# Kernel tuning notes

Measured on AMD Instinct MI355X. Metric: run time of the kernel, lower is better.

Reference implementation:

```python
import jax, jax.numpy as jnp
import numpy as np

EPS_LN = 1e-5

def _layernorm(x, g, b):
    mu = jnp.mean(x, axis=-1, keepdims=True)
    var = jnp.mean((x - mu) ** 2, axis=-1, keepdims=True)
    return (x - mu) * jax.lax.rsqrt(var + EPS_LN) * g + b


def setup_inputs() -> dict:
    B, S, D = 8, 2048, 512
    key = jax.random.key(0)
    ks = jax.random.split(key, 12)
    s = 1.0 / np.sqrt(D)
    inp = {
        "x": jax.random.normal(ks[0], (B, S, D), dtype=jnp.float32),
        "ln1_g": jnp.ones((D,), jnp.float32),
        "ln1_b": jnp.zeros((D,), jnp.float32),
        "ln2_g": jnp.ones((D,), jnp.float32),
        "ln2_b": jnp.zeros((D,), jnp.float32),
        "Wq": jax.random.normal(ks[1], (D, D), jnp.float32) * s,
        "bq": jnp.zeros((D,), jnp.float32),
        "Wk": jax.random.normal(ks[2], (D, D), jnp.float32) * s,
        "bk": jnp.zeros((D,), jnp.float32),
        "Wv": jax.random.normal(ks[3], (D, D), jnp.float32) * s,
        "bv": jnp.zeros((D,), jnp.float32),
        "Wi": jax.random.normal(ks[4], (D, D), jnp.float32) * s,
        "bi": jnp.zeros((D,), jnp.float32),
        "Wf": jax.random.normal(ks[5], (D, D), jnp.float32) * s,
        "bf": jnp.zeros((D,), jnp.float32),
        "Wo": jax.random.normal(ks[6], (D, D), jnp.float32) * s,
        "bo": jnp.zeros((D,), jnp.float32),
        "W1": jax.random.normal(ks[7], (D, 4 * D), jnp.float32) * s,
        "b1": jnp.zeros((4 * D,), jnp.float32),
        "W2": jax.random.normal(ks[8], (4 * D, D), jnp.float32) * (1.0 / np.sqrt(4 * D)),
        "b2": jnp.zeros((D,), jnp.float32),
    }
    return inp


def reference(x, ln1_g, ln1_b, ln2_g, ln2_b, Wq, bq, Wk, bk, Wv, bv,
              Wi, bi, Wf, bf, Wo, bo, W1, b1, W2, b2):
    B, S, D = x.shape
    normed = _layernorm(x, ln1_g, ln1_b)                      # [B,S,D]
    # All projections depend only on x -> batch them over time.
    q = normed @ Wq + bq
    k = (normed @ Wk + bk) / jnp.sqrt(jnp.float32(D))
    v = normed @ Wv + bv
    it = normed @ Wi + bi
    ft = normed @ Wf + bf
    o = jax.nn.sigmoid(normed @ Wo + bo)

    def tm(a):  # time-major [S,B,D]
        return jnp.swapaxes(a, 0, 1)

    def step(carry, xs):
        C, n, m = carry
        q_t, k_t, v_t, it_t, ft_t, o_t = xs
        m_new = jnp.maximum(ft_t + m, it_t)
        i_g = jnp.exp(it_t - m_new)
        f_g = jnp.exp(ft_t + m - m_new)
        # outer(v,k): [B,D,1]*[B,1,D]
        C_new = f_g[..., None] * C + i_g[..., None] * (v_t[:, :, None] * k_t[:, None, :])
        n_new = f_g * n + i_g * k_t
        h = o_t * jnp.einsum('bij,bj->bi', C_new, q_t)
        return (C_new, n_new, m_new), h

    C0 = jnp.zeros((B, D, D), x.dtype)
    n0 = jnp.zeros((B, D), x.dtype)
    m0 = jnp.zeros((B, D), x.dtype)
    (_, _, _), h_seq = jax.lax.scan(step, (C0, n0, m0),
                                    (tm(q), tm(k), tm(v), tm(it), tm(ft), tm(o)))
    h = jnp.swapaxes(h_seq, 0, 1)                             # [B,S,D]

    out = x + h
    ffn_in = _layernorm(out, ln2_g, ln2_b)
    ffn = jax.nn.gelu(ffn_in @ W1 + b1, approximate=False) @ W2 + b2
    return out + ffn
```

## Files before the change

kernel.cpp:

```cpp
#include <hip/hip_runtime.h>
#include <hip/hip_bf16.h>
#include <cstdint>

typedef unsigned short u16;
typedef unsigned int u32;
typedef __attribute__((ext_vector_type(8))) short short8;
typedef __attribute__((ext_vector_type(4))) float f32x4;

#define NB 8
#define NS 2048
#define ND 512
#define NM (NB * NS)
#define CL 64
#define NCH (NS / CL)
#define CL2 128
#define NCH2 (NS / CL2)
static constexpr size_t BSDn = (size_t)NM * ND;
#define KSCALE 0.044194173824159216f

#define OFF_QB ((size_t)0)
#define OFF_KB (BSDn * 2)
#define OFF_KT (BSDn * 4)
#define OFF_VT (BSDn * 6)
#define OFF_OT (BSDn * 8)
#define OFF_IT (BSDn * 10)
#define OFF_FT (BSDn * 14)
#define OFF_G  (BSDn * 18)
#define OFF_GO (BSDn * 18 + ((size_t)2 << 20))
#define OFF_AC (BSDn * 18 + ((size_t)3 << 20))
#define OFF_X  (OFF_AC + ((size_t)32 << 20))
#define OFF_UB (OFF_X + ((size_t)16 << 20))
#define OFF_GA (OFF_UB + ((size_t)16 << 20))
#define OFF_END (OFF_GA + ((size_t)1 << 20))

typedef __attribute__((address_space(1))) const u32 gas_u32;
typedef __attribute__((address_space(3))) u32 las_u32;

__device__ __forceinline__ u16 f2bf(float f) {
    u32 i = __builtin_bit_cast(u32, f);
    u32 r = i + 0x7FFFu + ((i >> 16) & 1u);
    return (u16)(r >> 16);
}
__device__ __forceinline__ float bf2f(u16 h) {
    return __builtin_bit_cast(float, (u32)h << 16);
}

__device__ __forceinline__ void lds_barrier() {
    __builtin_amdgcn_sched_barrier(0);
    asm volatile("s_waitcnt lgkmcnt(0)" ::: "memory");
    __builtin_amdgcn_s_barrier();
    __builtin_amdgcn_sched_barrier(0);
}

__global__ __launch_bounds__(256) void wcorr_kernel(
        const float* __restrict__ Wi, const float* __restrict__ Wf,
        u16* __restrict__ WT) {
    int idx = blockIdx.x * 256 + threadIdx.x;
    int n = idx / 1536, k = idx - n * 1536;
    const float* Wp = (n >> 9) ? Wf : Wi;
    int d = n & 511;
    u16 o;
    if (k < 1024) {
        o = f2bf(Wp[(size_t)(k & 511) * 512 + d]);
    } else {
        float w = Wp[(size_t)(k - 1024) * 512 + d];
        o = f2bf(w - bf2f(f2bf(w)));
    }
    WT[idx] = o;
}

__global__ __launch_bounds__(256) void wconv_kernel(const float* __restrict__ W,
        u16* __restrict__ WT, int lk, int N, int total) {
    int idx = blockIdx.x * 256 + threadIdx.x;
    if (idx >= total) return;
    int n = idx >> lk;
    int k = idx & ((1 << lk) - 1);
    WT[idx] = f2bf(W[(size_t)k * N + n]);
}

__global__ __launch_bounds__(256) void bias_concat_kernel(
        const float* b0, const float* b1, const float* b2,
        const float* b3, const float* b4, const float* b5,
        float* __restrict__ ball) {
    int idx = blockIdx.x * 256 + threadIdx.x;
    if (idx >= 3072) return;
    int p = idx >> 9, d = idx & 511;
    float v;
    switch (p) {
        case 0: v = b0[d]; break;
        case 1: v = b1[d]; break;
        case 2: v = b2[d]; break;
        case 3: v = b3[d]; break;
        case 4: v = b4[d]; break;
        default: v = b5[d]; break;
    }
    ball[idx] = v;
}

__global__ __launch_bounds__(256) void ln1_kernel(const float* __restrict__ x,
        const float* __restrict__ g, const float* __restrict__ bb,
        u16* __restrict__ nout) {
    int wave = threadIdx.x >> 6, lane = threadIdx.x & 63;
    size_t row = (size_t)blockIdx.x * 4 + wave;
    const float* xr = x + row * ND + lane * 8;
    float4 a0 = *(const float4*)xr;
    float4 a1 = *(const float4*)(xr + 4);
    float xs[8] = {a0.x, a0.y, a0.z, a0.w, a1.x, a1.y, a1.z, a1.w};
    float s = 0.f;
#pragma unroll
    for (int u = 0; u < 8; ++u) s += xs[u];
#pragma unroll
    for (int off = 32; off; off >>= 1) s += __shfl_xor(s, off);
    float mu = s * (1.0f / ND);
    float ss = 0.f;
#pragma unroll
    for (int u = 0; u < 8; ++u) { xs[u] -= mu; ss += xs[u] * xs[u]; }
#pragma unroll
    for (int off = 32; off; off >>= 1) ss += __shfl_xor(ss, off);
    float rs = rsqrtf(ss * (1.0f / ND) + 1e-5f);
    const float* gp = g + lane * 8;
    const float* bp = bb + lane * 8;
    float4 g0 = *(const float4*)gp, g1 = *(const float4*)(gp + 4);
    float4 c0 = *(const float4*)bp, c1 = *(const float4*)(bp + 4);
    float gg[8] = {g0.x, g0.y, g0.z, g0.w, g1.x, g1.y, g1.z, g1.w};
    float cc[8] = {c0.x, c0.y, c0.z, c0.w, c1.x, c1.y, c1.z, c1.w};
    u32 owh[4], owl[4];
#pragma unroll
    for (int u = 0; u < 4; ++u) {
        float y0 = xs[2 * u] * rs * gg[2 * u] + cc[2 * u];
        float y1 = xs[2 * u + 1] * rs * gg[2 * u + 1] + cc[2 * u + 1];
        u16 h0 = f2bf(y0), h1 = f2bf(y1);
        u16 l0 = f2bf(y0 - bf2f(h0)), l1 = f2bf(y1 - bf2f(h1));
        owh[u] = (u32)h0 | ((u32)h1 << 16);
        owl[u] = (u32)l0 | ((u32)l1 << 16);
    }
    u16* rb = nout + row * 1024;
    *(uint4*)(rb + lane * 8) = make_uint4(owh[0], owh[1], owh[2], owh[3]);
    *(uint4*)(rb + 512 + lane * 8) = make_uint4(owl[0], owl[1], owl[2], owl[3]);
}

__global__ __launch_bounds__(256) void resid_ln2_kernel(const float* __restrict__ x,
        const float* __restrict__ h, const float* __restrict__ g,
        const float* __restrict__ bb, float* __restrict__ outb,
        u16* __restrict__ fin) {
    int wave = threadIdx.x >> 6, lane = threadIdx.x & 63;
    size_t row = (size_t)blockIdx.x * 4 + wave;
    const float* xr = x + row * ND + lane * 8;
    const float* hr = h + row * ND + lane * 8;
    float4 a0 = *(const float4*)xr;
    float4 a1 = *(const float4*)(xr + 4);
    float4 h0 = *(const float4*)hr;
    float4 h1 = *(const float4*)(hr + 4);
    float xs[8] = {a0.x + h0.x, a0.y + h0.y, a0.z + h0.z, a0.w + h0.w,
                   a1.x + h1.x, a1.y + h1.y, a1.z + h1.z, a1.w + h1.w};
    float* orow = outb + row * ND + lane * 8;
    *(float4*)orow = make_float4(xs[0], xs[1], xs[2], xs[3]);
    *(float4*)(orow + 4) = make_float4(xs[4], xs[5], xs[6], xs[7]);
    float s = 0.f;
#pragma unroll
    for (int u = 0; u < 8; ++u) s += xs[u];
#pragma unroll
    for (int off = 32; off; off >>= 1) s += __shfl_xor(s, off);
    float mu = s * (1.0f / ND);
    float ss = 0.f;
#pragma unroll
    for (int u = 0; u < 8; ++u) { xs[u] -= mu; ss += xs[u] * xs[u]; }
#pragma unroll
    for (int off = 32; off; off >>= 1) ss += __shfl_xor(ss, off);
    float rs = rsqrtf(ss * (1.0f / ND) + 1e-5f);
    const float* gp = g + lane * 8;
    const float* bp = bb + lane * 8;
    float4 g0 = *(const float4*)gp, g1 = *(const float4*)(gp + 4);
    float4 c0 = *(const float4*)bp, c1 = *(const float4*)(bp + 4);
    float gg[8] = {g0.x, g0.y, g0.z, g0.w, g1.x, g1.y, g1.z, g1.w};
    float cc[8] = {c0.x, c0.y, c0.z, c0.w, c1.x, c1.y, c1.z, c1.w};
    u32 ow[4];
#pragma unroll
    for (int u = 0; u < 4; ++u) {
        float y0 = xs[2 * u] * rs * gg[2 * u] + cc[2 * u];
        float y1 = xs[2 * u + 1] * rs * gg[2 * u + 1] + cc[2 * u + 1];
        ow[u] = (u32)f2bf(y0) | ((u32)f2bf(y1) << 16);
    }
    *(uint4*)(fin + row * ND + lane * 8) = make_uint4(ow[0], ow[1], ow[2], ow[3]);
}

__global__ __launch_bounds__(256) void gqk_kernel(
        const u16* __restrict__ Qb, const u16* __restrict__ Kb,
        u16* __restrict__ Gm) {
    __shared__ u16 Qs[64][520];
    __shared__ u16 Ks[64][520];
    int tid = threadIdx.x;
    int w = tid >> 6, lane = tid & 63;
    int b = blockIdx.x >> 5, c = blockIdx.x & 31;
    int t0 = c * CL;
    {
        int row = tid >> 2, cb = (tid & 3) * 128;
        const u16* qsrc = Qb + ((size_t)b * NS + t0 + row) * ND + cb;
        const u16* ksrc = Kb + ((size_t)b * NS + t0 + row) * ND + cb;
#pragma unroll
        for (int u = 0; u < 16; ++u) {
            *(short8*)&Qs[row][cb + u * 8] = *(const short8*)(qsrc + u * 8);
            *(short8*)&Ks[row][cb + u * 8] = *(const short8*)(ksrc + u * 8);
        }
    }
    __syncthreads();
    int qw = lane & 15, kg = lane >> 4;
    f32x4 ga[4];
#pragma unroll
    for (int ns = 0; ns < 4; ++ns) ga[ns] = (f32x4){0.f, 0.f, 0.f, 0.f};
    for (int kb = 0; kb < 16; ++kb) {
        short8 aq = *(const short8*)&Qs[(w << 4) + qw][kb * 32 + (kg << 3)];
#pragma unroll
        for (int ns = 0; ns < 4; ++ns) {
            short8 bk = *(const short8*)&Ks[(ns << 4) + qw][kb * 32 + (kg << 3)];
            ga[ns] = __builtin_amdgcn_mfma_f32_16x16x32_bf16(aq, bk, ga[ns], 0, 0, 0);
        }
    }
    u16* gout = Gm + (size_t)(b * NCH + c) * CL * CL;
#pragma unroll
    for (int ns = 0; ns < 4; ++ns) {
#pragma unroll
        for (int rg = 0; rg < 4; ++rg) {
            int t = (w << 4) + (kg << 2) + rg;
            int s = (ns << 4) + qw;
            gout[t * CL + s] = (s <= t) ? f2bf(ga[ns][rg]) : (u16)0;
        }
    }
}

__global__ __launch_bounds__(256) void gqkoff_kernel(
        const u16* __restrict__ Qb, const u16* __restrict__ Kb,
        u16* __restrict__ Go) {
    __shared__ u16 Qs[64][520];
    __shared__ u16 Ks[64][520];
    int tid = threadIdx.x;
    int w = tid >> 6, lane = tid & 63;
    int b = blockIdx.x >> 4, c = blockIdx.x & 15;
    int t0q = c * CL2 + 64, t0k = c * CL2;
    {
        int row = tid >> 2, cb = (tid & 3) * 128;
        const u16* qsrc = Qb + ((size_t)b * NS + t0q + row) * ND + cb;
        const u16* ksrc = Kb + ((size_t)b * NS + t0k + row) * ND + cb;
#pragma unroll
        for (int u = 0; u < 16; ++u) {
            *(short8*)&Qs[row][cb + u * 8] = *(const short8*)(qsrc + u * 8);
            *(short8*)&Ks[row][cb + u * 8] = *(const short8*)(ksrc + u * 8);
        }
    }
    __syncthreads();
    int qw = lane & 15, kg = lane >> 4;
    f32x4 ga[4];
#pragma unroll
    for (int ns = 0; ns < 4; ++ns) ga[ns] = (f32x4){0.f, 0.f, 0.f, 0.f};
    for (int kb = 0; kb < 16; ++kb) {
        short8 aq = *(const short8*)&Qs[(w << 4) + qw][kb * 32 + (kg << 3)];
#pragma unroll
        for (int ns = 0; ns < 4; ++ns) {
            short8 bk = *(const short8*)&Ks[(ns << 4) + qw][kb * 32 + (kg << 3)];
            ga[ns] = __builtin_amdgcn_mfma_f32_16x16x32_bf16(aq, bk, ga[ns], 0, 0, 0);
        }
    }
    u16* gout = Go + (size_t)(b * NCH2 + c) * CL * CL;
#pragma unroll
    for (int ns = 0; ns < 4; ++ns) {
#pragma unroll
        for (int rg = 0; rg < 4; ++rg) {
            int t = (w << 4) + (kg << 2) + rg;
            int s = (ns << 4) + qw;
            gout[t * CL + s] = f2bf(ga[ns][rg]);
        }
    }
}

__global__ __launch_bounds__(128) void gates_kernel(
        const float* __restrict__ IT, const float* __restrict__ FT,
        const u16* __restrict__ VT,
        u16* __restrict__ A1g, u16* __restrict__ A2g,
        u16* __restrict__ Ubg, float* __restrict__ gamg) {
    int w = threadIdx.x >> 6, lane = threadIdx.x & 63;
    int rp = blockIdx.x & 7;
    int bl = blockIdx.x >> 3;
    int b = bl >> 5, isl = bl & 31;
    int il = rp * 2 + w;
    int i = (isl << 4) + il;
    size_t rowb = ((size_t)b * ND + i) * NS;
    size_t tb = (size_t)bl * 32768 + il * 128;
    float mo = 0.f;
    for (int c = 0; c < NCH2; ++c) {
        size_t g0 = rowb + c * CL2 + lane;
        float ft0 = FT[g0], it0 = IT[g0], v0 = bf2f(VT[g0]);
        float ft1 = FT[g0 + 64], it1 = IT[g0 + 64], v1 = bf2f(VT[g0 + 64]);
        float bs0 = ft0;
#pragma unroll
        for (int o = 1; o < 64; o <<= 1) {
            float nv = __shfl_up(bs0, o);
            if (lane >= o) bs0 += nv;
        }
        float e0 = it0 - bs0;
        float M0 = e0;
#pragma unroll
        for (int o = 1; o < 64; o <<= 1) {
            float nv = __shfl_up(M0, o);
            if (lane >= o) M0 = fmaxf(M0, nv);
        }
        M0 = fmaxf(M0, mo);
        float M0t = __shfl(M0, 63);
        float bs0t = __shfl(bs0, 63);
        float bs1 = ft1;
#pragma unroll
        for (int o = 1; o < 64; o <<= 1) {
            float nv = __shfl_up(bs1, o);
            if (lane >= o) bs1 += nv;
        }
        bs1 += bs0t;
        float e1 = it1 - bs1;
        float M1 = e1;
#pragma unroll
        for (int o = 1; o < 64; o <<= 1) {
            float nv = __shfl_up(M1, o);
            if (lane >= o) M1 = fmaxf(M1, nv);
        }
        M1 = fmaxf(M1, M0t);
        float E = __shfl(M1, 63);
        float bst = __shfl(bs1, 63);
        size_t oofs = tb + (size_t)c * 2048 + lane;
        Ubg[oofs] = f2bf(__expf(e0 - E) * v0);
        A1g[oofs] = f2bf(__expf(mo - M0));
        A2g[oofs] = f2bf(__expf(fminf(E - M0, 80.f)));
        Ubg[oofs + 64] = f2bf(__expf(e1 - E) * v1);
        A1g[oofs + 64] = f2bf(__expf(mo - M1));
        A2g[oofs + 64] = f2bf(__expf(fminf(E - M1, 80.f)));
        if (lane == 0) gamg[((size_t)bl * NCH2 + c) * 16 + il] = __expf(mo - E);
        mo = bst + E;
    }
}

__global__ __launch_bounds__(512) void recur_kernel(
        const u16* __restrict__ Qb, const u16* __restrict__ KT,
        const u16* __restrict__ Gd, const u16* __restrict__ Go,
        const u16* __restrict__ A1g, const u16* __restrict__ A2g,
        const u16* __restrict__ Ubg, const float* __restrict__ gamg,
        const u16* __restrict__ OT, float* __restrict__ H) {
    __shared__ u16 Chi[2][16][520];
    __shared__ u16 Ubl[2][16][136];
    __shared__ u16 A1l[2][16][136];
    __shared__ u16 A2l[2][16][136];
    __shared__ float gaml[2][16];
    int tid = threadIdx.x;
    int w = tid >> 6, lane = tid & 63;
    int hb = w >> 2, tl16 = w & 3;
    int b = blockIdx.x & 7;
    int isl = blockIdx.x >> 3;
    int i0 = isl << 4;
    int qw = lane & 15, kg = lane >> 4;
    f32x4 cacc[4];
#pragma unroll
    for (int n = 0; n < 4; ++n) cacc[n] = (f32x4){0.f, 0.f, 0.f, 0.f};

    size_t bT = (size_t)b * NS;
    size_t bD = (size_t)b * ND;
    size_t gt2 = (size_t)(b * 32 + isl) * 32768;
    int grow = tid >> 5;
    int gquad = (tid & 31) << 2;

    const u16* qpf = Qb + (bT + w * 16 + qw) * ND + (kg << 3);
    const u16* kpf = KT + (bD + w * 64 + qw) * NS + (kg << 3);
    const u16* gdp = Gd + ((size_t)(b * 32 + hb) * 4096)
                     + (size_t)(tl16 * 16 + qw) * 64 + (kg << 3);
    const u16* gop = Go + ((size_t)(b * 16) * 4096)
                     + (size_t)(tl16 * 16 + qw) * 64 + (kg << 3);
    const u16* ubp = Ubg + gt2 + grow * 128 + gquad;
    const u16* a1p = A1g + gt2 + grow * 128 + gquad;
    const u16* a2p = A2g + gt2 + grow * 128 + gquad;
    const float* gamp = gamg + (size_t)(b * 32 + isl) * (NCH2 * 16) + tid;
    const u16* otp = OT + (bD + i0 + qw) * NS + w * 16 + (kg << 2);

    uint2 nub = make_uint2(0, 0), na1 = make_uint2(0, 0), na2 = make_uint2(0, 0);
    float ngam = 0.f;
    auto issue_gates = [&]() {
        nub = *(const uint2*)ubp; ubp += 2048;
        na1 = *(const uint2*)a1p; a1p += 2048;
        na2 = *(const uint2*)a2p; a2p += 2048;
        if (tid < 16) ngam = *gamp;
        gamp += 16;
    };
    issue_gates();

    for (int c = 0; c < NCH2; ++c) {
        int buf = c & 1;
        int t0 = c * CL2;
        short8 nq[16], nk[16], ngd[2], ngo[2];
#pragma unroll
        for (int kk = 0; kk < 16; ++kk) nq[kk] = *(const short8*)(qpf + kk * 32);
        qpf += CL2 * ND;
#pragma unroll
        for (int kb = 0; kb < 4; ++kb)
#pragma unroll
            for (int n = 0; n < 4; ++n)
                nk[kb * 4 + n] = *(const short8*)(kpf + (size_t)(n << 4) * NS + kb * 32);
        kpf += CL2;
        ngd[0] = *(const short8*)gdp;
        ngd[1] = *(const short8*)(gdp + 32);
        gdp += 2 * 4096;
        if (hb == 1) {
            ngo[0] = *(const short8*)gop;
            ngo[1] = *(const short8*)(gop + 32);
        }
        gop += 4096;
        uint2 cov = *(const uint2*)otp;
        otp += CL2;
        uint2 cub = nub, ca1 = na1, ca2 = na2;
        float cgam = ngam;
        if (c + 1 < NCH2) issue_gates();

        *(uint2*)&Ubl[buf][grow][gquad] = cub;
        *(uint2*)&A1l[buf][grow][gquad] = ca1;
        *(uint2*)&A2l[buf][grow][gquad] = ca2;
        if (tid < 16) gaml[buf][tid] = cgam;
#pragma unroll
        for (int n = 0; n < 4; ++n) {
            int j = (w << 6) + (n << 4) + qw;
#pragma unroll
            for (int rg = 0; rg < 4; ++rg)
                Chi[buf][(kg << 2) + rg][j] = f2bf(cacc[n][rg]);
        }
        lds_barrier();

        f32x4 qc0 = (f32x4){0.f, 0.f, 0.f, 0.f};
        f32x4 qc1 = (f32x4){0.f, 0.f, 0.f, 0.f};
#pragma unroll
        for (int kk = 0; kk < 8; ++kk) {
            short8 b0 = *(const short8*)&Chi[buf][qw][(2 * kk) * 32 + (kg << 3)];
            short8 b1_ = *(const short8*)&Chi[buf][qw][(2 * kk + 1) * 32 + (kg << 3)];
            qc0 = __builtin_amdgcn_mfma_f32_16x16x32_bf16(nq[2 * kk], b0, qc0, 0, 0, 0);
            qc1 = __builtin_amdgcn_mfma_f32_16x16x32_bf16(nq[2 * kk + 1], b1_, qc1, 0, 0, 0);
        }
        f32x4 pin = (f32x4){0.f, 0.f, 0.f, 0.f};
        if (hb == 0) {
#pragma unroll
            for (int kb = 0; kb < 2; ++kb) {
                short8 bu = *(const short8*)&Ubl[buf][qw][kb * 32 + (kg << 3)];
                pin = __builtin_amdgcn_mfma_f32_16x16x32_bf16(ngd[kb], bu, pin, 0, 0, 0);
            }
        } else {
#pragma unroll
            for (int kb = 0; kb < 2; ++kb) {
                short8 bu = *(const short8*)&Ubl[buf][qw][kb * 32 + (kg << 3)];
                pin = __builtin_amdgcn_mfma_f32_16x16x32_bf16(ngo[kb], bu, pin, 0, 0, 0);
            }
#pragma unroll
            for (int kb = 0; kb < 2; ++kb) {
                short8 bu = *(const short8*)&Ubl[buf][qw][64 + kb * 32 + (kg << 3)];
                pin = __builtin_amdgcn_mfma_f32_16x16x32_bf16(ngd[kb], bu, pin, 0, 0, 0);
            }
        }
        {
            float g[4];
#pragma unroll
            for (int rg = 0; rg < 4; ++rg) g[rg] = gaml[buf][(kg << 2) + rg];
#pragma unroll
            for (int n = 0; n < 4; ++n) {
#pragma unroll
                for (int rg = 0; rg < 4; ++rg) cacc[n][rg] *= g[rg];
            }
#pragma unroll
            for (int kb = 0; kb < 4; ++kb) {
                short8 au = *(const short8*)&Ubl[buf][qw][kb * 32 + (kg << 3)];
#pragma unroll
                for (int n = 0; n < 4; ++n)
                    cacc[n] = __builtin_amdgcn_mfma_f32_16x16x32_bf16(
                            au, nk[kb * 4 + n], cacc[n], 0, 0, 0);
            }
        }
        {
            float ov[4];
            ov[0] = bf2f((u16)(cov.x & 0xffff));
            ov[1] = bf2f((u16)(cov.x >> 16));
            ov[2] = bf2f((u16)(cov.y & 0xffff));
            ov[3] = bf2f((u16)(cov.y >> 16));
#pragma unroll
            for (int rg = 0; rg < 4; ++rg) {
                int tl = w * 16 + (kg << 2) + rg;
                float a1v = bf2f(A1l[buf][qw][tl]);
                float a2v = bf2f(A2l[buf][qw][tl]);
                float qc = qc0[rg] + qc1[rg];
                H[(bT + t0 + tl) * ND + i0 + qw] = ov[rg] * (a1v * qc + a2v * pin[rg]);
            }
        }
    }
}

template <int MODE>
__global__ __launch_bounds__(256) void gemm_kernel(
        const u16* __restrict__ A, const u16* __restrict__ BT,
        int M, int N, int K, int lda, int ldb, int kwrap,
        const float* __restrict__ bias,
        char* __restrict__ pb,
        float* __restrict__ outf, u16* __restrict__ outh,
        const float* __restrict__ resid) {
    __shared__ u16 As[2][128 * 32];
    __shared__ u16 Bs[2][128 * 32];
    int tid = threadIdx.x;
    int wave = tid >> 6, lane = tid & 63;
    int wm = wave >> 1, wn = wave & 1;
    int m0 = blockIdx.y * 128;
    int n0 = blockIdx.x * 128;

    f32x4 acc[4][4];
#pragma unroll
    for (int fi = 0; fi < 4; ++fi)
#pragma unroll
        for (int fj = 0; fj < 4; ++fj)
            acc[fi][fj] = (f32x4){0.f, 0.f, 0.f, 0.f};

    int srow = lane >> 2;
    int slot = lane & 3;
    int r0s = wave * 32 + srow;
    int gs0 = (slot ^ ((r0s >> 1) & 3)) << 3;
    int gs1 = (slot ^ (((r0s + 16) >> 1) & 3)) << 3;
    const u16* Ag0 = A + (size_t)(m0 + r0s) * lda + gs0;
    const u16* Ag1 = A + (size_t)(m0 + r0s + 16) * lda + gs1;
    const u16* Bg0 = BT + (size_t)(n0 + r0s) * ldb + gs0;
    const u16* Bg1 = BT + (size_t)(n0 + r0s + 16) * ldb + gs1;
    int wl0 = wave * 32 * 32;
    int wl1 = wl0 + 16 * 32;

    int fr = lane & 15, kb = lane >> 4;
    int ra[4], rb4[4], sa[4], sb[4];
#pragma unroll
    for (int f = 0; f < 4; ++f) {
        ra[f] = wm * 64 + f * 16 + fr;
        rb4[f] = wn * 64 + f * 16 + fr;
        sa[f] = ra[f] * 32 + ((kb ^ ((ra[f] >> 1) & 3)) << 3);
        sb[f] = rb4[f] * 32 + ((kb ^ ((rb4[f] >> 1) & 3)) << 3);
    }

    int nk = K >> 5;
    __builtin_amdgcn_global_load_lds((gas_u32*)Ag0, (las_u32*)(&As[0][wl0]), 16, 0, 0);
    __builtin_amdgcn_global_load_lds((gas_u32*)Ag1, (las_u32*)(&As[0][wl1]), 16, 0, 0);
    __builtin_amdgcn_global_load_lds((gas_u32*)Bg0, (las_u32*)(&Bs[0][wl0]), 16, 0, 0);
    __builtin_amdgcn_global_load_lds((gas_u32*)Bg1, (las_u32*)(&Bs[0][wl1]), 16, 0, 0);
    __syncthreads();
#pragma unroll 2
    for (int t = 0; t < nk; ++t) {
        int cur = t & 1;
        if (t + 1 < nk) {
            int k0 = (t + 1) << 5;
            int ak0 = k0 - (k0 >= kwrap ? kwrap : 0);
            __builtin_amdgcn_global_load_lds((gas_u32*)(Ag0 + ak0), (las_u32*)(&As[cur ^ 1][wl0]), 16, 0, 0);
            __builtin_amdgcn_global_load_lds((gas_u32*)(Ag1 + ak0), (las_u32*)(&As[cur ^ 1][wl1]), 16, 0, 0);
            __builtin_amdgcn_global_load_lds((gas_u32*)(Bg0 + k0), (las_u32*)(&Bs[cur ^ 1][wl0]), 16, 0, 0);
            __builtin_amdgcn_global_load_lds((gas_u32*)(Bg1 + k0), (las_u32*)(&Bs[cur ^ 1][wl1]), 16, 0, 0);
        }
        short8 fa[4], fb[4];
#pragma unroll
        for (int f = 0; f < 4; ++f) {
            fa[f] = *(const short8*)(&As[cur][sa[f]]);
            fb[f] = *(const short8*)(&Bs[cur][sb[f]]);
        }
#pragma unroll
        for (int fi = 0; fi < 4; ++fi)
#pragma unroll
            for (int fj = 0; fj < 4; ++fj)
                acc[fi][fj] = __builtin_amdgcn_mfma_f32_16x16x32_bf16(
                        fa[fi], fb[fj], acc[fi][fj], 0, 0, 0);
        __syncthreads();
    }

    int rbase = (lane >> 4) * 4;
    int cbase = n0 + wn * 64 + (lane & 15);
#pragma unroll
    for (int fi = 0; fi < 4; ++fi) {
        int r0 = m0 + wm * 64 + fi * 16 + rbase;
#pragma unroll
        for (int fj = 0; fj < 4; ++fj) {
            int col = cbase + fj * 16;
            if (MODE == 0) {
                int p = col >> 9, d = col & 511;
                float bv_ = bias[col];
                float w0 = acc[fi][fj][0] + bv_;
                float w1 = acc[fi][fj][1] + bv_;
                float w2 = acc[fi][fj][2] + bv_;
                float w3 = acc[fi][fj][3] + bv_;
                size_t tb = ((size_t)(r0 >> 11) * ND + d) * NS + (r0 & 2047);
                if (p == 0) {
                    u16* q = (u16*)(pb + OFF_QB);
                    q[(size_t)(r0 + 0) * ND + d] = f2bf(w0);
                    q[(size_t)(r0 + 1) * ND + d] = f2bf(w1);
                    q[(size_t)(r0 + 2) * ND + d] = f2bf(w2);
                    q[(size_t)(r0 + 3) * ND + d] = f2bf(w3);
                } else if (p == 1) {
                    float s0 = w0 * KSCALE, s1 = w1 * KSCALE;
                    float s2 = w2 * KSCALE, s3 = w3 * KSCALE;
                    u16* kbuf = (u16*)(pb + OFF_KB);
                    kbuf[(size_t)(r0 + 0) * ND + d] = f2bf(s0);
                    kbuf[(size_t)(r0 + 1) * ND + d] = f2bf(s1);
                    kbuf[(size_t)(r0 + 2) * ND + d] = f2bf(s2);
                    kbuf[(size_t)(r0 + 3) * ND + d] = f2bf(s3);
                    uint2 wv = make_uint2((u32)f2bf(s0) | ((u32)f2bf(s1) << 16),
                                          (u32)f2bf(s2) | ((u32)f2bf(s3) << 16));
                    *(uint2*)((u16*)(pb + OFF_KT) + tb) = wv;
                } else if (p == 2) {
                    uint2 wv = make_uint2((u32)f2bf(w0) | ((u32)f2bf(w1) << 16),
                                          (u32)f2bf(w2) | ((u32)f2bf(w3) << 16));
                    *(uint2*)((u16*)(pb + OFF_VT) + tb) = wv;
                } else {
                    float s0 = 1.0f / (1.0f + __expf(-w0));
                    float s1 = 1.0f / (1.0f + __expf(-w1));
                    float s2 = 1.0f / (1.0f + __expf(-w2));
                    float s3 = 1.0f / (1.0f + __expf(-w3));
                    uint2 wv = make_uint2((u32)f2bf(s0) | ((u32)f2bf(s1) << 16),
                                          (u32)f2bf(s2) | ((u32)f2bf(s3) << 16));
                    *(uint2*)((u16*)(pb + OFF_OT) + tb) = wv;
                }
            } else if (MODE == 3) {
                int p = col >> 9, d = col & 511;
                float bv_ = bias[col];
                float w0 = acc[fi][fj][0] + bv_;
                float w1 = acc[fi][fj][1] + bv_;
                float w2 = acc[fi][fj][2] + bv_;
                float w3 = acc[fi][fj][3] + bv_;
                size_t tb = ((size_t)(r0 >> 11) * ND + d) * NS + (r0 & 2047);
                float* dst = (float*)(pb + (p == 0 ? OFF_IT : OFF_FT));
                *(float4*)(dst + tb) = make_float4(w0, w1, w2, w3);
            } else {
#pragma unroll
                for (int r = 0; r < 4; ++r) {
                    int row = r0 + r;
                    float v = acc[fi][fj][r];
                    if (MODE == 1) {
                        float val = v + bias[col];
                        val = 0.5f * val * (1.0f + erff(val * 0.70710678118654752f));
                        outh[(size_t)row * N + col] = f2bf(val);
                    } else {
                        float val = v + bias[col] + resid[(size_t)row * ND + col];
                        outf[(size_t)row * ND + col] = val;
                    }
                }
            }
        }
    }
}

extern "C" void kernel_launch(void* const* d_in, const int* in_sizes, int n_in,
                              void* d_out, int out_size, void* d_ws, size_t ws_size,
                              hipStream_t stream) {
    const float* x    = (const float*)d_in[0];
    const float* ln1g = (const float*)d_in[1];
    const float* ln1b = (const float*)d_in[2];
    const float* ln2g = (const float*)d_in[3];
    const float* ln2b = (const float*)d_in[4];
    const float* Wq = (const float*)d_in[5];
    const float* bq = (const float*)d_in[6];
    const float* Wk = (const float*)d_in[7];
    const float* bk = (const float*)d_in[8];
    const float* Wv = (const float*)d_in[9];
    const float* bv = (const float*)d_in[10];
    const float* Wi = (const float*)d_in[11];
    const float* bi = (const float*)d_in[12];
    const float* Wf = (const float*)d_in[13];
    const float* bfp = (const float*)d_in[14];
    const float* Wo = (const float*)d_in[15];
    const float* bo = (const float*)d_in[16];
    const float* W1 = (const float*)d_in[17];
    const float* b1 = (const float*)d_in[18];
    const float* W2 = (const float*)d_in[19];
    const float* b2 = (const float*)d_in[20];
    float* out = (float*)d_out;

    char* ws = (char*)d_ws;
    size_t off = 0;
    u16* W4T    = (u16*)(ws + off); off += (size_t)2048 * 512 * 2;
    u16* WcT    = (u16*)(ws + off); off += (size_t)1024 * 1536 * 2;
    u16* W1T    = (u16*)(ws + off); off += (size_t)2048 * 512 * 2;
    u16* W2T    = (u16*)(ws + off); off += (size_t)512 * 2048 * 2;
    float* ball = (float*)(ws + off); off += 3072 * 4;
    off = (off + 255) & ~(size_t)255;
    char* U = ws + off;
    u16*   Acorr = (u16*)(U + OFF_AC);
    float* Hbuf  = (float*)(U + OFF_AC);
    u16* ffnin = (u16*)U;
    u16* Gbuf  = (u16*)(U + OFF_KB);
    u16* A1g   = (u16*)(U + OFF_KB);
    u16* A2g   = (u16*)(U + OFF_X);
    u16* Ubg   = (u16*)(U + OFF_UB);
    float* gamg = (float*)(U + OFF_GA);
    size_t needed = (size_t)(U - ws) + OFF_END;
    if (ws_size < needed) return;

    wconv_kernel<<<1024, 256, 0, stream>>>(Wq, W4T, 9, 512, 512 * 512);
    wconv_kernel<<<1024, 256, 0, stream>>>(Wk, W4T + (size_t)512 * 512, 9, 512, 512 * 512);
    wconv_kernel<<<1024, 256, 0, stream>>>(Wv, W4T + (size_t)2 * 512 * 512, 9, 512, 512 * 512);
    wconv_kernel<<<1024, 256, 0, stream>>>(Wo, W4T + (size_t)3 * 512 * 512, 9, 512, 512 * 512);
    wcorr_kernel<<<(1024 * 1536) / 256, 256, 0, stream>>>(Wi, Wf, WcT);
    wconv_kernel<<<4096, 256, 0, stream>>>(W1, W1T, 9, 2048, 2048 * 512);
    wconv_kernel<<<4096, 256, 0, stream>>>(W2, W2T, 11, 512, 512 * 2048);
    bias_concat_kernel<<<12, 256, 0, stream>>>(bq, bk, bv, bo, bi, bfp, ball);

    ln1_kernel<<<NM / 4, 256, 0, stream>>>(x, ln1g, ln1b, Acorr);

    gemm_kernel<0><<<dim3(2048 / 128, NM / 128), 256, 0, stream>>>(
            Acorr, W4T, NM, 2048, 512, 1024, 512, 1 << 30, ball,
            U, nullptr, nullptr, nullptr);
    gemm_kernel<3><<<dim3(1024 / 128, NM / 128), 256, 0, stream>>>(
            Acorr, WcT, NM, 1024, 1536, 1024, 1536, 1024, ball + 2048,
            U, nullptr, nullptr, nullptr);

    gqk_kernel<<<NB * NCH, 256, 0, stream>>>(
            (const u16*)(U + OFF_QB), (const u16*)(U + OFF_KB), (u16*)(U + OFF_G));
    gqkoff_kernel<<<NB * NCH2, 256, 0, stream>>>(
            (const u16*)(U + OFF_QB), (const u16*)(U + OFF_KB), (u16*)(U + OFF_GO));

    gates_kernel<<<NB * 32 * 8, 128, 0, stream>>>(
            (const float*)(U + OFF_IT), (const float*)(U + OFF_FT),
            (const u16*)(U + OFF_VT), A1g, A2g, Ubg, gamg);

    recur_kernel<<<NB * 32, 512, 0, stream>>>(
            (const u16*)(U + OFF_QB), (const u16*)(U + OFF_KT),
            (const u16*)(U + OFF_G), (const u16*)(U + OFF_GO),
            A1g, A2g, Ubg, gamg, (const u16*)(U + OFF_OT), Hbuf);

    resid_ln2_kernel<<<NM / 4, 256, 0, stream>>>(x, Hbuf, ln2g, ln2b, out, ffnin);

    gemm_kernel<1><<<dim3(2048 / 128, NM / 128), 256, 0, stream>>>(
            ffnin, W1T, NM, 2048, 512, 512, 512, 1 << 30, b1,
            nullptr, nullptr, Gbuf, nullptr);

    gemm_kernel<2><<<dim3(512 / 128, NM / 128), 256, 0, stream>>>(
            Gbuf, W2T, NM, 512, 2048, 2048, 2048, 1 << 30, b2,
            nullptr, out, nullptr, out);

    (void)in_sizes; (void)n_in; (void)out_size; (void)ws_size;
}
```

Before: 569.3 us.

## Triple-buffer GEMM k-loop and merge prep and Gram kernels into single launches

New measurement: 528.5 us. 1.08x faster.

```diff
diff --git a/kernel.cpp b/kernel.cpp
--- a/kernel.cpp
+++ b/kernel.cpp
@@ -52,49 +52,61 @@
     __builtin_amdgcn_sched_barrier(0);
 }
 
-__global__ __launch_bounds__(256) void wcorr_kernel(
+__global__ __launch_bounds__(256) void prep_kernel(
+        const float* __restrict__ Wq, const float* __restrict__ Wk,
+        const float* __restrict__ Wv, const float* __restrict__ Wo,
         const float* __restrict__ Wi, const float* __restrict__ Wf,
-        u16* __restrict__ WT) {
-    int idx = blockIdx.x * 256 + threadIdx.x;
-    int n = idx / 1536, k = idx - n * 1536;
-    const float* Wp = (n >> 9) ? Wf : Wi;
-    int d = n & 511;
-    u16 o;
-    if (k < 1024) {
-        o = f2bf(Wp[(size_t)(k & 511) * 512 + d]);
+        const float* __restrict__ W1, const float* __restrict__ W2,
+        const float* __restrict__ bq, const float* __restrict__ bk,
+        const float* __restrict__ bv, const float* __restrict__ bo,
+        const float* __restrict__ bi, const float* __restrict__ bf_,
+        u16* __restrict__ W4T, u16* __restrict__ WcT,
+        u16* __restrict__ W1T, u16* __restrict__ W2T,
+        float* __restrict__ ball) {
+    int blk = blockIdx.x, tid = threadIdx.x;
+    if (blk < 4096) {
+        int idx = blk * 256 + tid;
+        int n = idx >> 9, k = idx & 511;
+        int p = n >> 9, d = n & 511;
+        const float* Wp = (p == 0) ? Wq : (p == 1) ? Wk : (p == 2) ? Wv : Wo;
+        W4T[idx] = f2bf(Wp[(size_t)k * 512 + d]);
+    } else if (blk < 10240) {
+        int idx = (blk - 4096) * 256 + tid;
+        int n = idx / 1536, k = idx - n * 1536;
+        const float* Wp = (n >> 9) ? Wf : Wi;
+        int d = n & 511;
+        u16 o;
+        if (k < 1024) {
+            o = f2bf(Wp[(size_t)(k & 511) * 512 + d]);
+        } else {
+            float w = Wp[(size_t)(k - 1024) * 512 + d];
+            o = f2bf(w - bf2f(f2bf(w)));
+        }
+        WcT[idx] = o;
+    } else if (blk < 14336) {
+        int idx = (blk - 10240) * 256 + tid;
+        int n = idx >> 9, k = idx & 511;
+        W1T[idx] = f2bf(W1[(size_t)k * 2048 + n]);
+    } else if (blk < 18432) {
+        int idx = (blk - 14336) * 256 + tid;
+        int n = idx >> 11, k = idx & 2047;
+        W2T[idx] = f2bf(W2[(size_t)k * 512 + n]);
     } else {
-        float w = Wp[(size_t)(k - 1024) * 512 + d];
-        o = f2bf(w - bf2f(f2bf(w)));
-    }
-    WT[idx] = o;
-}
-
-__global__ __launch_bounds__(256) void wconv_kernel(const float* __restrict__ W,
-        u16* __restrict__ WT, int lk, int N, int total) {
-    int idx = blockIdx.x * 256 + threadIdx.x;
-    if (idx >= total) return;
-    int n = idx >> lk;
-    int k = idx & ((1 << lk) - 1);
-    WT[idx] = f2bf(W[(size_t)k * N + n]);
-}
-
-__global__ __launch_bounds__(256) void bias_concat_kernel(
-        const float* b0, const float* b1, const float* b2,
-        const float* b3, const float* b4, const float* b5,
-        float* __restrict__ ball) {
-    int idx = blockIdx.x * 256 + threadIdx.x;
-    if (idx >= 3072) return;
-    int p = idx >> 9, d = idx & 511;
-    float v;
-    switch (p) {
-        case 0: v = b0[d]; break;
-        case 1: v = b1[d]; break;
-        case 2: v = b2[d]; break;
-        case 3: v = b3[d]; break;
-        case 4: v = b4[d]; break;
-        default: v = b5[d]; break;
-    }
-    ball[idx] = v;
+        int idx = (blk - 18432) * 256 + tid;
+        if (idx < 3072) {
+            int p = idx >> 9, d = idx & 511;
+            float v;
+            switch (p) {
+                case 0: v = bq[d]; break;
+                case 1: v = bk[d]; break;
+                case 2: v = bv[d]; break;
+                case 3: v = bo[d]; break;
+                case 4: v = bi[d]; break;
+                default: v = bf_[d]; break;
+            }
+            ball[idx] = v;
+        }
+    }
 }
 
 __global__ __launch_bounds__(256) void ln1_kernel(const float* __restrict__ x,
@@ -184,59 +196,32 @@
     *(uint4*)(fin + row * ND + lane * 8) = make_uint4(ow[0], ow[1], ow[2], ow[3]);
 }
 
-__global__ __launch_bounds__(256) void gqk_kernel(
+__global__ __launch_bounds__(256) void gqk2_kernel(
         const u16* __restrict__ Qb, const u16* __restrict__ Kb,
-        u16* __restrict__ Gm) {
+        u16* __restrict__ Gd, u16* __restrict__ Go) {
     __shared__ u16 Qs[64][520];
     __shared__ u16 Ks[64][520];
     int tid = threadIdx.x;
     int w = tid >> 6, lane = tid & 63;
-    int b = blockIdx.x >> 5, c = blockIdx.x & 31;
-    int t0 = c * CL;
-    {
-        int row = tid >> 2, cb = (tid & 3) * 128;
-        const u16* qsrc = Qb + ((size_t)b * NS + t0 + row) * ND + cb;
-        const u16* ksrc = Kb + ((size_t)b * NS + t0 + row) * ND + cb;
-#pragma unroll
-        for (int u = 0; u < 16; ++u) {
-            *(short8*)&Qs[row][cb + u * 8] = *(const short8*)(qsrc + u * 8);
-            *(short8*)&Ks[row][cb + u * 8] = *(const short8*)(ksrc + u * 8);
-        }
-    }
-    __syncthreads();
-    int qw = lane & 15, kg = lane >> 4;
-    f32x4 ga[4];
-#pragma unroll
-    for (int ns = 0; ns < 4; ++ns) ga[ns] = (f32x4){0.f, 0.f, 0.f, 0.f};
-    for (int kb = 0; kb < 16; ++kb) {
-        short8 aq = *(const short8*)&Qs[(w << 4) + qw][kb * 32 + (kg << 3)];
-#pragma unroll
-        for (int ns = 0; ns < 4; ++ns) {
-            short8 bk = *(const short8*)&Ks[(ns << 4) + qw][kb * 32 + (kg << 3)];
-            ga[ns] = __builtin_amdgcn_mfma_f32_16x16x32_bf16(aq, bk, ga[ns], 0, 0, 0);
-        }
-    }
-    u16* gout = Gm + (size_t)(b * NCH + c) * CL * CL;
-#pragma unroll
-    for (int ns = 0; ns < 4; ++ns) {
-#pragma unroll
-        for (int rg = 0; rg < 4; ++rg) {
-            int t = (w << 4) + (kg << 2) + rg;
-            int s = (ns << 4) + qw;
-            gout[t * CL + s] = (s <= t) ? f2bf(ga[ns][rg]) : (u16)0;
-        }
-    }
-}
-
-__global__ __launch_bounds__(256) void gqkoff_kernel(
-        const u16* __restrict__ Qb, const u16* __restrict__ Kb,
-        u16* __restrict__ Go) {
-    __shared__ u16 Qs[64][520];
-    __shared__ u16 Ks[64][520];
-    int tid = threadIdx.x;
-    int w = tid >> 6, lane = tid & 63;
-    int b = blockIdx.x >> 4, c = blockIdx.x & 15;
-    int t0q = c * CL2 + 64, t0k = c * CL2;
+    int blk = blockIdx.x;
+    int b, t0q, t0k;
+    bool masked;
+    u16* gout;
+    if (blk < 256) {
+        b = blk >> 5;
+        int c = blk & 31;
+        t0q = t0k = c * CL;
+        masked = true;
+        gout = Gd + (size_t)(b * NCH + c) * CL * CL;
+    } else {
+        int z = blk - 256;
+        b = z >> 4;
+        int c = z & 15;
+        t0q = c * CL2 + 64;
+        t0k = c * CL2;
+        masked = false;
+        gout = Go + (size_t)(b * NCH2 + c) * CL * CL;
+    }
     {
         int row = tid >> 2, cb = (tid & 3) * 128;
         const u16* qsrc = Qb + ((size_t)b * NS + t0q + row) * ND + cb;
@@ -260,14 +245,13 @@
             ga[ns] = __builtin_amdgcn_mfma_f32_16x16x32_bf16(aq, bk, ga[ns], 0, 0, 0);
         }
     }
-    u16* gout = Go + (size_t)(b * NCH2 + c) * CL * CL;
 #pragma unroll
     for (int ns = 0; ns < 4; ++ns) {
 #pragma unroll
         for (int rg = 0; rg < 4; ++rg) {
             int t = (w << 4) + (kg << 2) + rg;
             int s = (ns << 4) + qw;
-            gout[t * CL + s] = f2bf(ga[ns][rg]);
+            gout[t * CL + s] = (!masked || s <= t) ? f2bf(ga[ns][rg]) : (u16)0;
         }
     }
 }
@@ -498,8 +482,8 @@
         char* __restrict__ pb,
         float* __restrict__ outf, u16* __restrict__ outh,
         const float* __restrict__ resid) {
-    __shared__ u16 As[2][128 * 32];
-    __shared__ u16 Bs[2][128 * 32];
+    __shared__ u16 As[3][128 * 32];
+    __shared__ u16 Bs[3][128 * 32];
     int tid = threadIdx.x;
     int wave = tid >> 6, lane = tid & 63;
     int wm = wave >> 1, wn = wave & 1;
@@ -526,45 +510,55 @@
     int wl1 = wl0 + 16 * 32;
 
     int fr = lane & 15, kb = lane >> 4;
-    int ra[4], rb4[4], sa[4], sb[4];
+    int sa[4], sb[4];
 #pragma unroll
     for (int f = 0; f < 4; ++f) {
-        ra[f] = wm * 64 + f * 16 + fr;
-        rb4[f] = wn * 64 + f * 16 + fr;
-        sa[f] = ra[f] * 32 + ((kb ^ ((ra[f] >> 1) & 3)) << 3);
-        sb[f] = rb4[f] * 32 + ((kb ^ ((rb4[f] >> 1) & 3)) << 3);
+        int ra = wm * 64 + f * 16 + fr;
+        int rb = wn * 64 + f * 16 + fr;
+        sa[f] = ra * 32 + ((kb ^ ((ra >> 1) & 3)) << 3);
+        sb[f] = rb * 32 + ((kb ^ ((rb >> 1) & 3)) << 3);
     }
 
     int nk = K >> 5;
-    __builtin_amdgcn_global_load_lds((gas_u32*)Ag0, (las_u32*)(&As[0][wl0]), 16, 0, 0);
-    __builtin_amdgcn_global_load_lds((gas_u32*)Ag1, (las_u32*)(&As[0][wl1]), 16, 0, 0);
-    __builtin_amdgcn_global_load_lds((gas_u32*)Bg0, (las_u32*)(&Bs[0][wl0]), 16, 0, 0);
-    __builtin_amdgcn_global_load_lds((gas_u32*)Bg1, (las_u32*)(&Bs[0][wl1]), 16, 0, 0);
-    __syncthreads();
-#pragma unroll 2
+    auto STAGE = [&](int t, int bufi) {
+        int k0 = t << 5;
+        int ak0 = k0 - (k0 >= kwrap ? kwrap : 0);
+        __builtin_amdgcn_global_load_lds((gas_u32*)(Ag0 + ak0), (las_u32*)(&As[bufi][wl0]), 16, 0, 0);
+        __builtin_amdgcn_global_load_lds((gas_u32*)(Ag1 + ak0), (las_u32*)(&As[bufi][wl1]), 16, 0, 0);
+        __builtin_amdgcn_global_load_lds((gas_u32*)(Bg0 + k0), (las_u32*)(&Bs[bufi][wl0]), 16, 0, 0);
+        __builtin_amdgcn_global_load_lds((gas_u32*)(Bg1 + k0), (las_u32*)(&Bs[bufi][wl1]), 16, 0, 0);
+    };
+    STAGE(0, 0);
+    STAGE(1, 1);
+    int cur = 0;
+#pragma unroll 1
     for (int t = 0; t < nk; ++t) {
-        int cur = t & 1;
+        __builtin_amdgcn_sched_barrier(0);
         if (t + 1 < nk) {
-            int k0 = (t + 1) << 5;
-            int ak0 = k0 - (k0 >= kwrap ? kwrap : 0);
-            __builtin_amdgcn_global_load_lds((gas_u32*)(Ag0 + ak0), (las_u32*)(&As[cur ^ 1][wl0]), 16, 0, 0);
-            __builtin_amdgcn_global_load_lds((gas_u32*)(Ag1 + ak0), (las_u32*)(&As[cur ^ 1][wl1]), 16, 0, 0);
-            __builtin_amdgcn_global_load_lds((gas_u32*)(Bg0 + k0), (las_u32*)(&Bs[cur ^ 1][wl0]), 16, 0, 0);
-            __builtin_amdgcn_global_load_lds((gas_u32*)(Bg1 + k0), (las_u32*)(&Bs[cur ^ 1][wl1]), 16, 0, 0);
-        }
+            asm volatile("s_waitcnt vmcnt(4)" ::: "memory");
+        } else {
+            asm volatile("s_waitcnt vmcnt(0)" ::: "memory");
+        }
+        __builtin_amdgcn_s_barrier();
+        __builtin_amdgcn_sched_barrier(0);
         short8 fa[4], fb[4];
 #pragma unroll
         for (int f = 0; f < 4; ++f) {
             fa[f] = *(const short8*)(&As[cur][sa[f]]);
             fb[f] = *(const short8*)(&Bs[cur][sb[f]]);
         }
+        if (t + 2 < nk) {
+            int b2 = cur - 1;
+            if (b2 < 0) b2 += 3;
+            STAGE(t + 2, b2);
+        }
 #pragma unroll
         for (int fi = 0; fi < 4; ++fi)
 #pragma unroll
             for (int fj = 0; fj < 4; ++fj)
                 acc[fi][fj] = __builtin_amdgcn_mfma_f32_16x16x32_bf16(
                         fa[fi], fb[fj], acc[fi][fj], 0, 0, 0);
-        __syncthreads();
+        cur = (cur == 2) ? 0 : cur + 1;
     }
 
     int rbase = (lane >> 4) * 4;
@@ -688,14 +682,9 @@
     size_t needed = (size_t)(U - ws) + OFF_END;
     if (ws_size < needed) return;
 
-    wconv_kernel<<<1024, 256, 0, stream>>>(Wq, W4T, 9, 512, 512 * 512);
-    wconv_kernel<<<1024, 256, 0, stream>>>(Wk, W4T + (size_t)512 * 512, 9, 512, 512 * 512);
-    wconv_kernel<<<1024, 256, 0, stream>>>(Wv, W4T + (size_t)2 * 512 * 512, 9, 512, 512 * 512);
-    wconv_kernel<<<1024, 256, 0, stream>>>(Wo, W4T + (size_t)3 * 512 * 512, 9, 512, 512 * 512);
-    wcorr_kernel<<<(1024 * 1536) / 256, 256, 0, stream>>>(Wi, Wf, WcT);
-    wconv_kernel<<<4096, 256, 0, stream>>>(W1, W1T, 9, 2048, 2048 * 512);
-    wconv_kernel<<<4096, 256, 0, stream>>>(W2, W2T, 11, 512, 512 * 2048);
-    bias_concat_kernel<<<12, 256, 0, stream>>>(bq, bk, bv, bo, bi, bfp, ball);
+    prep_kernel<<<18444, 256, 0, stream>>>(
+            Wq, Wk, Wv, Wo, Wi, Wf, W1, W2,
+            bq, bk, bv, bo, bi, bfp, W4T, WcT, W1T, W2T, ball);
 
     ln1_kernel<<<NM / 4, 256, 0, stream>>>(x, ln1g, ln1b, Acorr);
 
@@ -706,10 +695,9 @@
             Acorr, WcT, NM, 1024, 1536, 1024, 1536, 1024, ball + 2048,
             U, nullptr, nullptr, nullptr);
 
-    gqk_kernel<<<NB * NCH, 256, 0, stream>>>(
-            (const u16*)(U + OFF_QB), (const u16*)(U + OFF_KB), (u16*)(U + OFF_G));
-    gqkoff_kernel<<<NB * NCH2, 256, 0, stream>>>(
-            (const u16*)(U + OFF_QB), (const u16*)(U + OFF_KB), (u16*)(U + OFF_GO));
+    gqk2_kernel<<<NB * NCH + NB * NCH2, 256, 0, stream>>>(
+            (const u16*)(U + OFF_QB), (const u16*)(U + OFF_KB),
+            (u16*)(U + OFF_G), (u16*)(U + OFF_GO));
 
     gates_kernel<<<NB * 32 * 8, 128, 0, stream>>>(
             (const float*)(U + OFF_IT), (const float*)(U + OFF_FT),
```
